# Performance work log

Measured on AMD Instinct MI355X. Metric: run time of the kernel, lower is better.

## Reference

```python
import jax, jax.numpy as jnp
import numpy as np

B = 8192      # batch
LAT = 256     # latent_dimension
HID = 512     # hidden_size
INP = 128     # input_size (n_layer_types + 1 feature)
T = 64        # max_length
MLP = 512     # fixed MLP width in source


def _lin(key, fan_in, fan_out):
    kw, kb = jax.random.split(key)
    s = 1.0 / np.sqrt(fan_in)
    W = jax.random.uniform(kw, (fan_in, fan_out), jnp.float32, -s, s)
    b = jax.random.uniform(kb, (fan_out,), jnp.float32, -s, s)
    return W, b


def setup_inputs() -> dict:
    key = jax.random.key(0)
    ks = jax.random.split(key, 16)
    x = jax.random.normal(ks[0], (B, LAT), jnp.float32)
    W1, b1 = _lin(ks[1], LAT, MLP)
    W2, b2 = _lin(ks[2], MLP, MLP)
    W3, b3 = _lin(ks[3], MLP, MLP)
    Wh1, bh1 = _lin(ks[4], MLP, MLP)
    Wh2, bh2 = _lin(ks[5], MLP, HID)
    Wc1, bc1 = _lin(ks[6], MLP, MLP)
    Wc2, bc2 = _lin(ks[7], MLP, HID)
    Wx1, bx1 = _lin(ks[8], MLP, MLP)
    Wx2, bx2 = _lin(ks[9], MLP, INP)
    Wih, bih = _lin(ks[10], INP, 4 * HID)   # LSTM input->gates (i,f,g,o)
    Whh, bhh = _lin(ks[11], HID, 4 * HID)   # LSTM hidden->gates
    Wp, bp = _lin(ks[12], HID, INP)          # predictor head
    return dict(x=x, W1=W1, b1=b1, W2=W2, b2=b2, W3=W3, b3=b3,
                Wh1=Wh1, bh1=bh1, Wh2=Wh2, bh2=bh2,
                Wc1=Wc1, bc1=bc1, Wc2=Wc2, bc2=bc2,
                Wx1=Wx1, bx1=bx1, Wx2=Wx2, bx2=bx2,
                Wih=Wih, bih=bih, Whh=Whh, bhh=bhh, Wp=Wp, bp=bp)


def _lrelu(v):
    return jnp.where(v >= 0, v, 0.2 * v)


def _head(v):
    # split [d-1, 1]: softmax over layer types, sigmoid on feature scalar
    lt = jax.nn.softmax(v[..., :-1], axis=-1)
    ft = jax.nn.sigmoid(v[..., -1:])
    return jnp.concatenate([lt, ft], axis=-1)


def reference(x, W1, b1, W2, b2, W3, b3, Wh1, bh1, Wh2, bh2,
              Wc1, bc1, Wc2, bc2, Wx1, bx1, Wx2, bx2,
              Wih, bih, Whh, bhh, Wp, bp):
    z = _lrelu(x @ W1 + b1)
    z = _lrelu(z @ W2 + b2)
    z = _lrelu(z @ W3 + b3)
    h = _lrelu(z @ Wh1 + bh1) @ Wh2 + bh2          # [B, HID]
    c = _lrelu(z @ Wc1 + bc1) @ Wc2 + bc2          # [B, HID]
    x0 = _head(_lrelu(z @ Wx1 + bx1) @ Wx2 + bx2)  # [B, INP]

    def step(carry, _):
        xt, h, c = carry
        g = xt @ Wih + h @ Whh + (bih + bhh)        # [B, 4*HID]
        i, f, gg, o = jnp.split(g, 4, axis=-1)      # torch gate order i,f,g,o
        c2 = jax.nn.sigmoid(f) * c + jax.nn.sigmoid(i) * jnp.tanh(gg)
        h2 = jax.nn.sigmoid(o) * jnp.tanh(c2)
        nxt = _head(h2 @ Wp + bp)
        return (nxt, h2, c2), nxt

    # The torch loop reruns the LSTM over the growing prefix with the same
    # initial (h,c) and takes the last output; by LSTM causality this equals
    _, ys = jax.lax.scan(step, (x0, h, c), None, length=T)
    return jnp.transpose(ys, (1, 0, 2))  # [B, T, INP]
```

## Files before the change

kernel.cpp:

```cpp
#include <hip/hip_runtime.h>


typedef _Float16 h16;
typedef __attribute__((ext_vector_type(8))) _Float16 f16x8;
typedef __attribute__((ext_vector_type(4))) float f32x4;

#define BB 8192
#define TT 64

__device__ __forceinline__ void gload16(const void* g, void* lds) {
  __builtin_amdgcn_global_load_lds(
      (const __attribute__((address_space(1))) unsigned int*)g,
      (__attribute__((address_space(3))) unsigned int*)lds, 16, 0, 0);
}

__device__ __forceinline__ float sigm(float x) { return 1.f / (1.f + __expf(-x)); }
__device__ __forceinline__ float tanhf_(float x) { return 2.f / (1.f + __expf(-2.f * x)) - 1.f; }

enum { EP_LRELU = 0, EP_LIN16 = 1, EP_F32 = 2, EP_LSTM = 3 };

template <int EP>
__global__ __launch_bounds__(256) void gemm128(
    const h16* __restrict__ A, int lda, const h16* __restrict__ Bt,
    const float* __restrict__ bias, int K,
    h16* __restrict__ out16, int ldo, int ocol,
    float* __restrict__ outf, int ldf,
    float* __restrict__ Cbuf, h16* __restrict__ Hout) {
  __shared__ h16 As[128 * 64];
  __shared__ h16 Bs[128 * 64];
  const int tid = threadIdx.x;
  const int lane = tid & 63;
  const int w = tid >> 6;
  const int m0 = blockIdx.x * 128;
  const int n0 = blockIdx.y * 128;

  f32x4 acc[4][4];
#pragma unroll
  for (int i = 0; i < 4; ++i)
#pragma unroll
    for (int j = 0; j < 4; ++j) acc[i][j] = (f32x4)0.f;

  const int rh = (w >> 1) * 64;
  const int arow = lane & 15;
  const int khi = lane >> 4;

  const int nkt = K >> 6;
  for (int kt = 0; kt < nkt; ++kt) {
#pragma unroll
    for (int li = 0; li < 4; ++li) {
      int L = w * 4 + li;
      int r = L * 8 + (lane >> 3);
      int c = lane & 7;
      int gc = c ^ (r & 7);
      gload16(A + (size_t)(m0 + r) * lda + kt * 64 + gc * 8, &As[L * 512]);
      gload16(Bt + (size_t)(n0 + r) * K + kt * 64 + gc * 8, &Bs[L * 512]);
    }
    __syncthreads();
#pragma unroll
    for (int kk = 0; kk < 2; ++kk) {
      const int kc = kk * 4 + khi;
      f16x8 af[4], bf[4];
#pragma unroll
      for (int mt = 0; mt < 4; ++mt) {
        int r = rh + mt * 16 + arow;
        af[mt] = *(const f16x8*)&As[r * 64 + (kc ^ (r & 7)) * 8];
      }
#pragma unroll
      for (int j = 0; j < 4; ++j) {
        int nt = (EP == EP_LSTM) ? (j * 2 + (w & 1)) : ((w & 1) * 4 + j);
        int r = nt * 16 + arow;
        bf[j] = *(const f16x8*)&Bs[r * 64 + (kc ^ (r & 7)) * 8];
      }
#pragma unroll
      for (int mt = 0; mt < 4; ++mt)
#pragma unroll
        for (int j = 0; j < 4; ++j)
          acc[mt][j] =
              __builtin_amdgcn_mfma_f32_16x16x32_f16(af[mt], bf[j], acc[mt][j], 0, 0, 0);
    }
    __syncthreads();
  }

  if constexpr (EP == EP_LSTM) {
    const int jj = (w & 1) * 16 + arow;
    const int j = blockIdx.y * 32 + jj;
    const float bI = bias[n0 + 0 * 32 + jj];
    const float bF = bias[n0 + 1 * 32 + jj];
    const float bG = bias[n0 + 2 * 32 + jj];
    const float bO = bias[n0 + 3 * 32 + jj];
#pragma unroll
    for (int mt = 0; mt < 4; ++mt) {
#pragma unroll
      for (int r = 0; r < 4; ++r) {
        int m = m0 + rh + mt * 16 + khi * 4 + r;
        float gi = sigm(acc[mt][0][r] + bI);
        float gf = sigm(acc[mt][1][r] + bF);
        float gg = tanhf_(acc[mt][2][r] + bG);
        float go = sigm(acc[mt][3][r] + bO);
        size_t ci = (size_t)m * 512 + j;
        float c2 = gf * Cbuf[ci] + gi * gg;
        Cbuf[ci] = c2;
        Hout[(size_t)m * 640 + 128 + j] = (h16)(go * tanhf_(c2));
      }
    }
  } else {
#pragma unroll
    for (int mt = 0; mt < 4; ++mt) {
#pragma unroll
      for (int j = 0; j < 4; ++j) {
        int nt = (w & 1) * 4 + j;
        int n = n0 + nt * 16 + arow;
        float bv = bias[n];
#pragma unroll
        for (int r = 0; r < 4; ++r) {
          int m = m0 + rh + mt * 16 + khi * 4 + r;
          float v = acc[mt][j][r] + bv;
          if constexpr (EP == EP_LRELU) {
            v = v >= 0.f ? v : 0.2f * v;
            out16[(size_t)m * ldo + n] = (h16)v;
          } else if constexpr (EP == EP_LIN16) {
            out16[(size_t)m * ldo + ocol + n] = (h16)v;
          } else {
            outf[(size_t)m * ldf + n] = v;
          }
        }
      }
    }
  }
}

__global__ __launch_bounds__(256) void head_gemm(
    const h16* __restrict__ A, int lda, const h16* __restrict__ Bt,
    const float* __restrict__ bias, int K, h16* __restrict__ Xout,
    float* __restrict__ ydst, int tstep) {
  __shared__ h16 As[64 * 64];
  __shared__ h16 Bs[128 * 64];
  const int tid = threadIdx.x;
  const int lane = tid & 63;
  const int w = tid >> 6;
  const int m0 = blockIdx.x * 64;
  const int arow = lane & 15;
  const int khi = lane >> 4;

  f32x4 acc[8];
#pragma unroll
  for (int j = 0; j < 8; ++j) acc[j] = (f32x4)0.f;

  const int nkt = K >> 6;
  for (int kt = 0; kt < nkt; ++kt) {
#pragma unroll
    for (int li = 0; li < 2; ++li) {
      int L = w * 2 + li;
      int r = L * 8 + (lane >> 3);
      int c = lane & 7;
      int gc = c ^ (r & 7);
      gload16(A + (size_t)(m0 + r) * lda + kt * 64 + gc * 8, &As[L * 512]);
    }
#pragma unroll
    for (int li = 0; li < 4; ++li) {
      int L = w * 4 + li;
      int r = L * 8 + (lane >> 3);
      int c = lane & 7;
      int gc = c ^ (r & 7);
      gload16(Bt + (size_t)r * K + kt * 64 + gc * 8, &Bs[L * 512]);
    }
    __syncthreads();
#pragma unroll
    for (int kk = 0; kk < 2; ++kk) {
      int kc = kk * 4 + khi;
      int ra = w * 16 + arow;
      f16x8 af = *(const f16x8*)&As[ra * 64 + (kc ^ (ra & 7)) * 8];
#pragma unroll
      for (int nt = 0; nt < 8; ++nt) {
        int rb = nt * 16 + arow;
        f16x8 bf = *(const f16x8*)&Bs[rb * 64 + (kc ^ (rb & 7)) * 8];
        acc[nt] = __builtin_amdgcn_mfma_f32_16x16x32_f16(af, bf, acc[nt], 0, 0, 0);
      }
    }
    __syncthreads();
  }

#pragma unroll
  for (int r = 0; r < 4; ++r) {
    int m = m0 + w * 16 + khi * 4 + r;
    float v[8];
    float mx = -1e30f;
#pragma unroll
    for (int nt = 0; nt < 8; ++nt) {
      int col = nt * 16 + arow;
      v[nt] = acc[nt][r] + bias[col];
      if (col != 127) mx = fmaxf(mx, v[nt]);
    }
#pragma unroll
    for (int s = 1; s < 16; s <<= 1) mx = fmaxf(mx, __shfl_xor(mx, s, 16));
    float sm = 0.f;
#pragma unroll
    for (int nt = 0; nt < 8; ++nt) {
      int col = nt * 16 + arow;
      if (col != 127) sm += __expf(v[nt] - mx);
    }
#pragma unroll
    for (int s = 1; s < 16; s <<= 1) sm += __shfl_xor(sm, s, 16);
    float inv = 1.f / sm;
#pragma unroll
    for (int nt = 0; nt < 8; ++nt) {
      int col = nt * 16 + arow;
      float res = (col == 127) ? sigm(v[nt]) : __expf(v[nt] - mx) * inv;
      Xout[(size_t)m * 640 + col] = (h16)res;
      if (ydst) ydst[((size_t)m * 64 + tstep) * 128 + col] = res;
    }
  }
}

__global__ void cvt16(const float* __restrict__ in, h16* __restrict__ out, int n) {
  int i = blockIdx.x * 256 + threadIdx.x;
  if (i < n) out[i] = (h16)in[i];
}

__global__ void transposeW(const float* __restrict__ W, h16* __restrict__ WT, int K,
                           int N) {
  int i = blockIdx.x * 256 + threadIdx.x;
  if (i >= K * N) return;
  int k = i / N, n = i % N;
  WT[(size_t)n * K + k] = (h16)W[i];
}

__global__ void prep_gate(const float* __restrict__ Wih, const float* __restrict__ Whh,
                          const float* __restrict__ bih, const float* __restrict__ bhh,
                          h16* __restrict__ WgT, float* __restrict__ bg) {
  int i = blockIdx.x * 256 + threadIdx.x;
  if (i >= 2048 * 640) return;
  int np = i / 640, k = i % 640;
  int tn = np >> 7, q = (np >> 5) & 3, jj = np & 31;
  int orig = q * 512 + tn * 32 + jj;
  float wv = (k < 128) ? Wih[(size_t)k * 2048 + orig]
                       : Whh[(size_t)(k - 128) * 2048 + orig];
  WgT[i] = (h16)wv;
  if (k == 0) bg[np] = bih[orig] + bhh[orig];
}

extern "C" void kernel_launch(void* const* d_in, const int* in_sizes, int n_in,
                              void* d_out, int out_size, void* d_ws, size_t ws_size,
                              hipStream_t stream) {
  const float* x = (const float*)d_in[0];
  const float* W1 = (const float*)d_in[1];
  const float* b1 = (const float*)d_in[2];
  const float* W2 = (const float*)d_in[3];
  const float* b2 = (const float*)d_in[4];
  const float* W3 = (const float*)d_in[5];
  const float* b3 = (const float*)d_in[6];
  const float* Wh1 = (const float*)d_in[7];
  const float* bh1 = (const float*)d_in[8];
  const float* Wh2 = (const float*)d_in[9];
  const float* bh2 = (const float*)d_in[10];
  const float* Wc1 = (const float*)d_in[11];
  const float* bc1 = (const float*)d_in[12];
  const float* Wc2 = (const float*)d_in[13];
  const float* bc2 = (const float*)d_in[14];
  const float* Wx1 = (const float*)d_in[15];
  const float* bx1 = (const float*)d_in[16];
  const float* Wx2 = (const float*)d_in[17];
  const float* bx2 = (const float*)d_in[18];
  const float* Wih = (const float*)d_in[19];
  const float* bih = (const float*)d_in[20];
  const float* Whh = (const float*)d_in[21];
  const float* bhh = (const float*)d_in[22];
  const float* Wp = (const float*)d_in[23];
  const float* bp = (const float*)d_in[24];

  char* ws = (char*)d_ws;
  size_t off = 0;
  auto take = [&](size_t bytes) -> void* {
    void* p = ws + off;
    off += (bytes + 255) & ~(size_t)255;
    return p;
  };
  h16* X16 = (h16*)take((size_t)BB * 256 * 2);
  h16* Za = (h16*)take((size_t)BB * 512 * 2);
  h16* Zb = (h16*)take((size_t)BB * 512 * 2);
  h16* XHa = (h16*)take((size_t)BB * 640 * 2);
  h16* XHb = (h16*)take((size_t)BB * 640 * 2);
  float* C = (float*)take((size_t)BB * 512 * 4);
  h16* W1T = (h16*)take(256 * 512 * 2);
  h16* W2T = (h16*)take(512 * 512 * 2);
  h16* W3T = (h16*)take(512 * 512 * 2);
  h16* Wh1T = (h16*)take(512 * 512 * 2);
  h16* Wh2T = (h16*)take(512 * 512 * 2);
  h16* Wc1T = (h16*)take(512 * 512 * 2);
  h16* Wc2T = (h16*)take(512 * 512 * 2);
  h16* Wx1T = (h16*)take(512 * 512 * 2);
  h16* Wx2T = (h16*)take(128 * 512 * 2);
  h16* WpT = (h16*)take(128 * 512 * 2);
  h16* WgT = (h16*)take((size_t)2048 * 640 * 2);
  float* bg = (float*)take(2048 * 4);

  dim3 blk(256);
  cvt16<<<(BB * 256 + 255) / 256, blk, 0, stream>>>(x, X16, BB * 256);
  transposeW<<<(256 * 512 + 255) / 256, blk, 0, stream>>>(W1, W1T, 256, 512);
  transposeW<<<(512 * 512 + 255) / 256, blk, 0, stream>>>(W2, W2T, 512, 512);
  transposeW<<<(512 * 512 + 255) / 256, blk, 0, stream>>>(W3, W3T, 512, 512);
  transposeW<<<(512 * 512 + 255) / 256, blk, 0, stream>>>(Wh1, Wh1T, 512, 512);
  transposeW<<<(512 * 512 + 255) / 256, blk, 0, stream>>>(Wh2, Wh2T, 512, 512);
  transposeW<<<(512 * 512 + 255) / 256, blk, 0, stream>>>(Wc1, Wc1T, 512, 512);
  transposeW<<<(512 * 512 + 255) / 256, blk, 0, stream>>>(Wc2, Wc2T, 512, 512);
  transposeW<<<(512 * 512 + 255) / 256, blk, 0, stream>>>(Wx1, Wx1T, 512, 512);
  transposeW<<<(512 * 128 + 255) / 256, blk, 0, stream>>>(Wx2, Wx2T, 512, 128);
  transposeW<<<(512 * 128 + 255) / 256, blk, 0, stream>>>(Wp, WpT, 512, 128);
  prep_gate<<<(2048 * 640 + 255) / 256, blk, 0, stream>>>(Wih, Whh, bih, bhh, WgT, bg);

  gemm128<EP_LRELU><<<dim3(64, 4), blk, 0, stream>>>(X16, 256, W1T, b1, 256, Za, 512, 0,
                                                     nullptr, 0, nullptr, nullptr);
  gemm128<EP_LRELU><<<dim3(64, 4), blk, 0, stream>>>(Za, 512, W2T, b2, 512, Zb, 512, 0,
                                                     nullptr, 0, nullptr, nullptr);
  gemm128<EP_LRELU><<<dim3(64, 4), blk, 0, stream>>>(Zb, 512, W3T, b3, 512, Za, 512, 0,
                                                     nullptr, 0, nullptr, nullptr);
  gemm128<EP_LRELU><<<dim3(64, 4), blk, 0, stream>>>(Za, 512, Wh1T, bh1, 512, Zb, 512, 0,
                                                     nullptr, 0, nullptr, nullptr);
  gemm128<EP_LIN16><<<dim3(64, 4), blk, 0, stream>>>(Zb, 512, Wh2T, bh2, 512, XHa, 640,
                                                     128, nullptr, 0, nullptr, nullptr);
  gemm128<EP_LRELU><<<dim3(64, 4), blk, 0, stream>>>(Za, 512, Wc1T, bc1, 512, Zb, 512, 0,
                                                     nullptr, 0, nullptr, nullptr);
  gemm128<EP_F32><<<dim3(64, 4), blk, 0, stream>>>(Zb, 512, Wc2T, bc2, 512, nullptr, 0, 0,
                                                   C, 512, nullptr, nullptr);
  gemm128<EP_LRELU><<<dim3(64, 4), blk, 0, stream>>>(Za, 512, Wx1T, bx1, 512, Zb, 512, 0,
                                                     nullptr, 0, nullptr, nullptr);
  head_gemm<<<128, blk, 0, stream>>>(Zb, 512, Wx2T, bx2, 512, XHa, nullptr, 0);

  float* yout = (float*)d_out;
  for (int t = 0; t < TT; ++t) {
    h16* in_ = (t & 1) ? XHb : XHa;
    h16* out_ = (t & 1) ? XHa : XHb;
    gemm128<EP_LSTM><<<dim3(64, 16), blk, 0, stream>>>(in_, 640, WgT, bg, 640, nullptr,
                                                       0, 0, nullptr, 0, C, out_);
    head_gemm<<<128, blk, 0, stream>>>(out_ + 128, 640, WpT, bp, 512, out_, yout, t);
  }
}
```

Before: 3.353 ms.

## Replace LSTM gate GEMM with 256x256 double-buffered 8-wave pipelined kernel

Introduces a dedicated gate8 kernel for the per-step LSTM gate GEMM. It uses 256x256 tiles, 512 threads, double-buffered LDS staging via global_load_lds, fine-grained barriers with explicit vmcnt waits, and MFMA priority raising so loads overlap with matrix math. The gate weight permutation is reordered to fit the new tile and wave mapping. The head GEMM is also made double-buffered. This trades a much larger LDS footprint and fewer blocks (256 per step) for better reuse and latency hiding, and hand-tuned wait counts risk subtle races.

```diff
diff --git a/kernel.cpp b/kernel.cpp
--- a/kernel.cpp
+++ b/kernel.cpp
@@ -17,17 +17,274 @@
 __device__ __forceinline__ float sigm(float x) { return 1.f / (1.f + __expf(-x)); }
 __device__ __forceinline__ float tanhf_(float x) { return 2.f / (1.f + __expf(-2.f * x)) - 1.f; }
 
-enum { EP_LRELU = 0, EP_LIN16 = 1, EP_F32 = 2, EP_LSTM = 3 };
+#define MIDBAR_LG()                                        \
+  do {                                                     \
+    __builtin_amdgcn_s_barrier();                          \
+    asm volatile("s_waitcnt lgkmcnt(0)" ::: "memory");     \
+    __builtin_amdgcn_sched_barrier(0);                     \
+  } while (0)
+#define ENDBAR()                                           \
+  do {                                                     \
+    __builtin_amdgcn_s_barrier();                          \
+    asm volatile("" ::: "memory");                         \
+  } while (0)
+
+__global__ __launch_bounds__(512, 2) void gate8(
+    const h16* __restrict__ A, const h16* __restrict__ Bt,
+    const float* __restrict__ bg, float* __restrict__ Cbuf,
+    h16* __restrict__ Hout) {
+  __shared__ __align__(16) h16 As[2][256 * 64];
+  __shared__ __align__(16) h16 Bs[2][256 * 64];
+  const int tid = threadIdx.x;
+  const int lane = tid & 63;
+  const int wid = tid >> 6;
+  const int wr = wid >> 2, wc = wid & 3;
+  const int m0 = blockIdx.x * 256;
+  const int n0 = blockIdx.y * 256;
+  const int arow = lane & 15, khi = lane >> 4;
+  const int x7 = arow & 7;
+
+  auto stage = [&](h16(*dst)[256 * 64], int slot, int h, const h16* src,
+                   int base, int kt) {
+#pragma unroll
+    for (int li = 0; li < 2; ++li) {
+      int rowbase = li * 128 + h * 64 + wid * 8;
+      int row = rowbase + (lane >> 3);
+      int gc = (lane & 7) ^ (lane >> 3);
+      gload16(src + (size_t)(base + row) * 640 + kt * 64 + gc * 8,
+              &dst[slot][rowbase * 64]);
+    }
+  };
+
+  f32x4 acc[8][4];
+#pragma unroll
+  for (int i = 0; i < 8; ++i)
+#pragma unroll
+    for (int j = 0; j < 4; ++j) acc[i][j] = (f32x4)0.f;
+  f16x8 af[4], bf[2][4];
+
+  auto readA = [&](int slot, int ms, int ks) {
+#pragma unroll
+    for (int mr = 0; mr < 4; ++mr) {
+      int r = wr * 128 + ms * 64 + mr * 16 + arow;
+      af[mr] = *(const f16x8*)&As[slot][r * 64 + ((ks * 4 + khi) ^ x7) * 8];
+    }
+  };
+  auto readB = [&](int slot, int ks) {
+#pragma unroll
+    for (int j = 0; j < 4; ++j) {
+      int rb = wc * 64 + j * 16 + arow;
+      bf[ks][j] = *(const f16x8*)&Bs[slot][rb * 64 + ((ks * 4 + khi) ^ x7) * 8];
+    }
+  };
+  auto mfma16 = [&](int ms, int ks) {
+    __builtin_amdgcn_s_setprio(1);
+#pragma unroll
+    for (int mr = 0; mr < 4; ++mr)
+#pragma unroll
+      for (int j = 0; j < 4; ++j)
+        acc[ms * 4 + mr][j] = __builtin_amdgcn_mfma_f32_16x16x32_f16(
+            af[mr], bf[ks][j], acc[ms * 4 + mr][j], 0, 0, 0);
+    __builtin_amdgcn_s_setprio(0);
+  };
+
+  stage(Bs, 0, 0, Bt, n0, 0);
+  stage(Bs, 0, 1, Bt, n0, 0);
+  stage(As, 0, 0, A, m0, 0);
+  stage(As, 0, 1, A, m0, 0);
+  stage(Bs, 1, 0, Bt, n0, 1);
+  stage(Bs, 1, 1, Bt, n0, 1);
+  stage(As, 1, 0, A, m0, 1);
+  asm volatile("s_waitcnt vmcnt(6)" ::: "memory");
+  ENDBAR();
+
+#pragma unroll 1
+  for (int i = 0; i < 5; ++i) {
+    const int t2 = 2 * i + 2, t3 = 2 * i + 3;
+    readB(0, 0);
+    readB(0, 1);
+    readA(0, 0, 0);
+    stage(As, 1, 1, A, m0, 2 * i + 1);
+    MIDBAR_LG();
+    mfma16(0, 0);
+    ENDBAR();
+    readA(0, 0, 1);
+    if (t2 < 10) stage(Bs, 0, 0, Bt, n0, t2);
+    MIDBAR_LG();
+    mfma16(0, 1);
+    ENDBAR();
+    readA(0, 1, 0);
+    if (t2 < 10) stage(Bs, 0, 1, Bt, n0, t2);
+    MIDBAR_LG();
+    mfma16(1, 0);
+    ENDBAR();
+    readA(0, 1, 1);
+    if (t2 < 10) stage(As, 0, 0, A, m0, t2);
+    if (i < 4)
+      asm volatile("s_waitcnt vmcnt(6)" ::: "memory");
+    else
+      asm volatile("s_waitcnt vmcnt(0)" ::: "memory");
+    MIDBAR_LG();
+    mfma16(1, 1);
+    ENDBAR();
+    readB(1, 0);
+    readB(1, 1);
+    readA(1, 0, 0);
+    if (t2 < 10) stage(As, 0, 1, A, m0, t2);
+    MIDBAR_LG();
+    mfma16(0, 0);
+    ENDBAR();
+    readA(1, 0, 1);
+    if (t3 < 10) stage(Bs, 1, 0, Bt, n0, t3);
+    MIDBAR_LG();
+    mfma16(0, 1);
+    ENDBAR();
+    readA(1, 1, 0);
+    if (t3 < 10) stage(Bs, 1, 1, Bt, n0, t3);
+    MIDBAR_LG();
+    mfma16(1, 0);
+    ENDBAR();
+    readA(1, 1, 1);
+    if (t3 < 10) stage(As, 1, 0, A, m0, t3);
+    if (i < 4)
+      asm volatile("s_waitcnt vmcnt(6)" ::: "memory");
+    else
+      asm volatile("s_waitcnt vmcnt(0)" ::: "memory");
+    MIDBAR_LG();
+    mfma16(1, 1);
+    ENDBAR();
+  }
+
+  const int hj = blockIdx.y * 64 + wc * 16 + arow;
+  const int nb = n0 + wc * 64;
+  const float bI = bg[nb + arow];
+  const float bF = bg[nb + 16 + arow];
+  const float bG = bg[nb + 32 + arow];
+  const float bO = bg[nb + 48 + arow];
+#pragma unroll
+  for (int mrep = 0; mrep < 8; ++mrep) {
+#pragma unroll
+    for (int r = 0; r < 4; ++r) {
+      int m = m0 + wr * 128 + mrep * 16 + khi * 4 + r;
+      float gi = sigm(acc[mrep][0][r] + bI);
+      float gf = sigm(acc[mrep][1][r] + bF);
+      float gg = tanhf_(acc[mrep][2][r] + bG);
+      float go = sigm(acc[mrep][3][r] + bO);
+      size_t ci = (size_t)m * 512 + hj;
+      float c2 = gf * Cbuf[ci] + gi * gg;
+      Cbuf[ci] = c2;
+      Hout[(size_t)m * 640 + 128 + hj] = (h16)(go * tanhf_(c2));
+    }
+  }
+}
+
+__global__ __launch_bounds__(256) void head_gemm2(
+    const h16* __restrict__ A, int lda, const h16* __restrict__ Bt,
+    const float* __restrict__ bias, int nkt, h16* __restrict__ Xout,
+    float* __restrict__ ydst, int tstep) {
+  __shared__ __align__(16) h16 As[2][64 * 64];
+  __shared__ __align__(16) h16 Bs[2][128 * 64];
+  const int tid = threadIdx.x;
+  const int lane = tid & 63;
+  const int w = tid >> 6;
+  const int m0 = blockIdx.x * 64;
+  const int arow = lane & 15, khi = lane >> 4;
+  const int x7 = arow & 7;
+
+  auto stageA = [&](int slot, int kt) {
+#pragma unroll
+    for (int li = 0; li < 2; ++li) {
+      int rowbase = li * 32 + w * 8;
+      int row = rowbase + (lane >> 3);
+      int gc = (lane & 7) ^ (lane >> 3);
+      gload16(A + (size_t)(m0 + row) * lda + kt * 64 + gc * 8,
+              &As[slot][rowbase * 64]);
+    }
+  };
+  auto stageB = [&](int slot, int kt) {
+#pragma unroll
+    for (int li = 0; li < 4; ++li) {
+      int rowbase = li * 32 + w * 8;
+      int row = rowbase + (lane >> 3);
+      int gc = (lane & 7) ^ (lane >> 3);
+      gload16(Bt + (size_t)row * 512 + kt * 64 + gc * 8,
+              &Bs[slot][rowbase * 64]);
+    }
+  };
+
+  f32x4 acc[8];
+#pragma unroll
+  for (int j = 0; j < 8; ++j) acc[j] = (f32x4)0.f;
+
+  stageA(0, 0);
+  stageB(0, 0);
+#pragma unroll 1
+  for (int kt = 0; kt < nkt; ++kt) {
+    int p = kt & 1;
+    if (kt + 1 < nkt) {
+      stageA(p ^ 1, kt + 1);
+      stageB(p ^ 1, kt + 1);
+      asm volatile("s_waitcnt vmcnt(6)" ::: "memory");
+    } else {
+      asm volatile("s_waitcnt vmcnt(0)" ::: "memory");
+    }
+    ENDBAR();
+#pragma unroll
+    for (int kk = 0; kk < 2; ++kk) {
+      int kc = kk * 4 + khi;
+      int ra = w * 16 + arow;
+      f16x8 afr = *(const f16x8*)&As[p][ra * 64 + (kc ^ x7) * 8];
+#pragma unroll
+      for (int nt = 0; nt < 8; ++nt) {
+        int rb = nt * 16 + arow;
+        f16x8 bfr = *(const f16x8*)&Bs[p][rb * 64 + (kc ^ x7) * 8];
+        acc[nt] = __builtin_amdgcn_mfma_f32_16x16x32_f16(afr, bfr, acc[nt], 0, 0, 0);
+      }
+    }
+    ENDBAR();
+  }
+
+#pragma unroll
+  for (int r = 0; r < 4; ++r) {
+    int m = m0 + w * 16 + khi * 4 + r;
+    float v[8];
+    float mx = -1e30f;
+#pragma unroll
+    for (int nt = 0; nt < 8; ++nt) {
+      int col = nt * 16 + arow;
+      v[nt] = acc[nt][r] + bias[col];
+      if (col != 127) mx = fmaxf(mx, v[nt]);
+    }
+#pragma unroll
+    for (int s = 1; s < 16; s <<= 1) mx = fmaxf(mx, __shfl_xor(mx, s, 16));
+    float sm = 0.f;
+#pragma unroll
+    for (int nt = 0; nt < 8; ++nt) {
+      int col = nt * 16 + arow;
+      if (col != 127) sm += __expf(v[nt] - mx);
+    }
+#pragma unroll
+    for (int s = 1; s < 16; s <<= 1) sm += __shfl_xor(sm, s, 16);
+    float inv = 1.f / sm;
+#pragma unroll
+    for (int nt = 0; nt < 8; ++nt) {
+      int col = nt * 16 + arow;
+      float res = (col == 127) ? sigm(v[nt]) : __expf(v[nt] - mx) * inv;
+      Xout[(size_t)m * 640 + col] = (h16)res;
+      if (ydst) ydst[((size_t)m * 64 + tstep) * 128 + col] = res;
+    }
+  }
+}
+
+enum { EP_LRELU = 0, EP_LIN16 = 1, EP_F32 = 2 };
 
 template <int EP>
 __global__ __launch_bounds__(256) void gemm128(
     const h16* __restrict__ A, int lda, const h16* __restrict__ Bt,
-    const float* __restrict__ bias, int K,
-    h16* __restrict__ out16, int ldo, int ocol,
-    float* __restrict__ outf, int ldf,
-    float* __restrict__ Cbuf, h16* __restrict__ Hout) {
-  __shared__ h16 As[128 * 64];
-  __shared__ h16 Bs[128 * 64];
+    const float* __restrict__ bias, int K, h16* __restrict__ out16, int ldo,
+    int ocol, float* __restrict__ outf, int ldf) {
+  __shared__ __align__(16) h16 As[128 * 64];
+  __shared__ __align__(16) h16 Bs[128 * 64];
   const int tid = threadIdx.x;
   const int lane = tid & 63;
   const int w = tid >> 6;
@@ -67,7 +324,7 @@
       }
 #pragma unroll
       for (int j = 0; j < 4; ++j) {
-        int nt = (EP == EP_LSTM) ? (j * 2 + (w & 1)) : ((w & 1) * 4 + j);
+        int nt = (w & 1) * 4 + j;
         int r = nt * 16 + arow;
         bf[j] = *(const f16x8*)&Bs[r * 64 + (kc ^ (r & 7)) * 8];
       }
@@ -81,133 +338,26 @@
     __syncthreads();
   }
 
-  if constexpr (EP == EP_LSTM) {
-    const int jj = (w & 1) * 16 + arow;
-    const int j = blockIdx.y * 32 + jj;
-    const float bI = bias[n0 + 0 * 32 + jj];
-    const float bF = bias[n0 + 1 * 32 + jj];
-    const float bG = bias[n0 + 2 * 32 + jj];
-    const float bO = bias[n0 + 3 * 32 + jj];
-#pragma unroll
-    for (int mt = 0; mt < 4; ++mt) {
+#pragma unroll
+  for (int mt = 0; mt < 4; ++mt) {
+#pragma unroll
+    for (int j = 0; j < 4; ++j) {
+      int nt = (w & 1) * 4 + j;
+      int n = n0 + nt * 16 + arow;
+      float bv = bias[n];
 #pragma unroll
       for (int r = 0; r < 4; ++r) {
         int m = m0 + rh + mt * 16 + khi * 4 + r;
-        float gi = sigm(acc[mt][0][r] + bI);
-        float gf = sigm(acc[mt][1][r] + bF);
-        float gg = tanhf_(acc[mt][2][r] + bG);
-        float go = sigm(acc[mt][3][r] + bO);
-        size_t ci = (size_t)m * 512 + j;
-        float c2 = gf * Cbuf[ci] + gi * gg;
-        Cbuf[ci] = c2;
-        Hout[(size_t)m * 640 + 128 + j] = (h16)(go * tanhf_(c2));
-      }
-    }
-  } else {
-#pragma unroll
-    for (int mt = 0; mt < 4; ++mt) {
-#pragma unroll
-      for (int j = 0; j < 4; ++j) {
-        int nt = (w & 1) * 4 + j;
-        int n = n0 + nt * 16 + arow;
-        float bv = bias[n];
-#pragma unroll
-        for (int r = 0; r < 4; ++r) {
-          int m = m0 + rh + mt * 16 + khi * 4 + r;
-          float v = acc[mt][j][r] + bv;
-          if constexpr (EP == EP_LRELU) {
-            v = v >= 0.f ? v : 0.2f * v;
-            out16[(size_t)m * ldo + n] = (h16)v;
-          } else if constexpr (EP == EP_LIN16) {
-            out16[(size_t)m * ldo + ocol + n] = (h16)v;
-          } else {
-            outf[(size_t)m * ldf + n] = v;
-          }
+        float v = acc[mt][j][r] + bv;
+        if constexpr (EP == EP_LRELU) {
+          v = v >= 0.f ? v : 0.2f * v;
+          out16[(size_t)m * ldo + n] = (h16)v;
+        } else if constexpr (EP == EP_LIN16) {
+          out16[(size_t)m * ldo + ocol + n] = (h16)v;
+        } else {
+          outf[(size_t)m * ldf + n] = v;
         }
       }
-    }
-  }
-}
-
-__global__ __launch_bounds__(256) void head_gemm(
-    const h16* __restrict__ A, int lda, const h16* __restrict__ Bt,
-    const float* __restrict__ bias, int K, h16* __restrict__ Xout,
-    float* __restrict__ ydst, int tstep) {
-  __shared__ h16 As[64 * 64];
-  __shared__ h16 Bs[128 * 64];
-  const int tid = threadIdx.x;
-  const int lane = tid & 63;
-  const int w = tid >> 6;
-  const int m0 = blockIdx.x * 64;
-  const int arow = lane & 15;
-  const int khi = lane >> 4;
-
-  f32x4 acc[8];
-#pragma unroll
-  for (int j = 0; j < 8; ++j) acc[j] = (f32x4)0.f;
-
-  const int nkt = K >> 6;
-  for (int kt = 0; kt < nkt; ++kt) {
-#pragma unroll
-    for (int li = 0; li < 2; ++li) {
-      int L = w * 2 + li;
-      int r = L * 8 + (lane >> 3);
-      int c = lane & 7;
-      int gc = c ^ (r & 7);
-      gload16(A + (size_t)(m0 + r) * lda + kt * 64 + gc * 8, &As[L * 512]);
-    }
-#pragma unroll
-    for (int li = 0; li < 4; ++li) {
-      int L = w * 4 + li;
-      int r = L * 8 + (lane >> 3);
-      int c = lane & 7;
-      int gc = c ^ (r & 7);
-      gload16(Bt + (size_t)r * K + kt * 64 + gc * 8, &Bs[L * 512]);
-    }
-    __syncthreads();
-#pragma unroll
-    for (int kk = 0; kk < 2; ++kk) {
-      int kc = kk * 4 + khi;
-      int ra = w * 16 + arow;
-      f16x8 af = *(const f16x8*)&As[ra * 64 + (kc ^ (ra & 7)) * 8];
-#pragma unroll
-      for (int nt = 0; nt < 8; ++nt) {
-        int rb = nt * 16 + arow;
-        f16x8 bf = *(const f16x8*)&Bs[rb * 64 + (kc ^ (rb & 7)) * 8];
-        acc[nt] = __builtin_amdgcn_mfma_f32_16x16x32_f16(af, bf, acc[nt], 0, 0, 0);
-      }
-    }
-    __syncthreads();
-  }
-
-#pragma unroll
-  for (int r = 0; r < 4; ++r) {
-    int m = m0 + w * 16 + khi * 4 + r;
-    float v[8];
-    float mx = -1e30f;
-#pragma unroll
-    for (int nt = 0; nt < 8; ++nt) {
-      int col = nt * 16 + arow;
-      v[nt] = acc[nt][r] + bias[col];
-      if (col != 127) mx = fmaxf(mx, v[nt]);
-    }
-#pragma unroll
-    for (int s = 1; s < 16; s <<= 1) mx = fmaxf(mx, __shfl_xor(mx, s, 16));
-    float sm = 0.f;
-#pragma unroll
-    for (int nt = 0; nt < 8; ++nt) {
-      int col = nt * 16 + arow;
-      if (col != 127) sm += __expf(v[nt] - mx);
-    }
-#pragma unroll
-    for (int s = 1; s < 16; s <<= 1) sm += __shfl_xor(sm, s, 16);
-    float inv = 1.f / sm;
-#pragma unroll
-    for (int nt = 0; nt < 8; ++nt) {
-      int col = nt * 16 + arow;
-      float res = (col == 127) ? sigm(v[nt]) : __expf(v[nt] - mx) * inv;
-      Xout[(size_t)m * 640 + col] = (h16)res;
-      if (ydst) ydst[((size_t)m * 64 + tstep) * 128 + col] = res;
     }
   }
 }
@@ -231,8 +381,8 @@
   int i = blockIdx.x * 256 + threadIdx.x;
   if (i >= 2048 * 640) return;
   int np = i / 640, k = i % 640;
-  int tn = np >> 7, q = (np >> 5) & 3, jj = np & 31;
-  int orig = q * 512 + tn * 32 + jj;
+  int by = np >> 8, wcc = (np >> 6) & 3, q = (np >> 4) & 3, jj = np & 15;
+  int orig = q * 512 + by * 64 + wcc * 16 + jj;
   float wv = (k < 128) ? Wih[(size_t)k * 2048 + orig]
                        : Whh[(size_t)(k - 128) * 2048 + orig];
   WgT[i] = (h16)wv;
@@ -308,30 +458,21 @@
   transposeW<<<(512 * 128 + 255) / 256, blk, 0, stream>>>(Wp, WpT, 512, 128);
   prep_gate<<<(2048 * 640 + 255) / 256, blk, 0, stream>>>(Wih, Whh, bih, bhh, WgT, bg);
 
-  gemm128<EP_LRELU><<<dim3(64, 4), blk, 0, stream>>>(X16, 256, W1T, b1, 256, Za, 512, 0,
-                                                     nullptr, 0, nullptr, nullptr);
-  gemm128<EP_LRELU><<<dim3(64, 4), blk, 0, stream>>>(Za, 512, W2T, b2, 512, Zb, 512, 0,
-                                                     nullptr, 0, nullptr, nullptr);
-  gemm128<EP_LRELU><<<dim3(64, 4), blk, 0, stream>>>(Zb, 512, W3T, b3, 512, Za, 512, 0,
-                                                     nullptr, 0, nullptr, nullptr);
-  gemm128<EP_LRELU><<<dim3(64, 4), blk, 0, stream>>>(Za, 512, Wh1T, bh1, 512, Zb, 512, 0,
-                                                     nullptr, 0, nullptr, nullptr);
-  gemm128<EP_LIN16><<<dim3(64, 4), blk, 0, stream>>>(Zb, 512, Wh2T, bh2, 512, XHa, 640,
-                                                     128, nullptr, 0, nullptr, nullptr);
-  gemm128<EP_LRELU><<<dim3(64, 4), blk, 0, stream>>>(Za, 512, Wc1T, bc1, 512, Zb, 512, 0,
-                                                     nullptr, 0, nullptr, nullptr);
-  gemm128<EP_F32><<<dim3(64, 4), blk, 0, stream>>>(Zb, 512, Wc2T, bc2, 512, nullptr, 0, 0,
-                                                   C, 512, nullptr, nullptr);
-  gemm128<EP_LRELU><<<dim3(64, 4), blk, 0, stream>>>(Za, 512, Wx1T, bx1, 512, Zb, 512, 0,
-                                                     nullptr, 0, nullptr, nullptr);
-  head_gemm<<<128, blk, 0, stream>>>(Zb, 512, Wx2T, bx2, 512, XHa, nullptr, 0);
+  gemm128<EP_LRELU><<<dim3(64, 4), blk, 0, stream>>>(X16, 256, W1T, b1, 256, Za, 512, 0, nullptr, 0);
+  gemm128<EP_LRELU><<<dim3(64, 4), blk, 0, stream>>>(Za, 512, W2T, b2, 512, Zb, 512, 0, nullptr, 0);
+  gemm128<EP_LRELU><<<dim3(64, 4), blk, 0, stream>>>(Zb, 512, W3T, b3, 512, Za, 512, 0, nullptr, 0);
+  gemm128<EP_LRELU><<<dim3(64, 4), blk, 0, stream>>>(Za, 512, Wh1T, bh1, 512, Zb, 512, 0, nullptr, 0);
+  gemm128<EP_LIN16><<<dim3(64, 4), blk, 0, stream>>>(Zb, 512, Wh2T, bh2, 512, XHa, 640, 128, nullptr, 0);
+  gemm128<EP_LRELU><<<dim3(64, 4), blk, 0, stream>>>(Za, 512, Wc1T, bc1, 512, Zb, 512, 0, nullptr, 0);
+  gemm128<EP_F32><<<dim3(64, 4), blk, 0, stream>>>(Zb, 512, Wc2T, bc2, 512, nullptr, 0, 0, C, 512);
+  gemm128<EP_LRELU><<<dim3(64, 4), blk, 0, stream>>>(Za, 512, Wx1T, bx1, 512, Zb, 512, 0, nullptr, 0);
+  head_gemm2<<<128, blk, 0, stream>>>(Zb, 512, Wx2T, bx2, 8, XHa, nullptr, 0);
 
   float* yout = (float*)d_out;
   for (int t = 0; t < TT; ++t) {
     h16* in_ = (t & 1) ? XHb : XHa;
     h16* out_ = (t & 1) ? XHa : XHb;
-    gemm128<EP_LSTM><<<dim3(64, 16), blk, 0, stream>>>(in_, 640, WgT, bg, 640, nullptr,
-                                                       0, 0, nullptr, 0, C, out_);
-    head_gemm<<<128, blk, 0, stream>>>(out_ + 128, 640, WpT, bp, 512, out_, yout, t);
-  }
-}
+    gate8<<<dim3(32, 8), dim3(512), 0, stream>>>(in_, WgT, bg, C, out_);
+    head_gemm2<<<128, blk, 0, stream>>>(out_ + 128, 640, WpT, bp, 8, out_, yout, t);
+  }
+}
```

New measurement: 2.970 ms. 1.13x faster.
